# Optimization experiments

Measured on AMD Instinct MI355X. Metric: run time of the kernel, lower is better.

Reference implementation:

```python
import jax, jax.numpy as jnp
import numpy as np


def setup_inputs() -> dict:
    key = jax.random.key(0)
    k1, k2 = jax.random.split(key)
    B, C, H, W = 64, 64, 32, 32
    ROWS, COLS, O, KH, KW = 28, 28, 128, 5, 5
    x = jax.random.normal(k1, (B, C, H, W), dtype=jnp.float32)
    weight = jax.random.normal(k2, (ROWS, COLS, O, C, KH, KW), dtype=jnp.float32) * 0.05
    return {"x": x, "weight": weight}


def reference(x, weight):
    # Locally-connected conv (unshared weights), stride 1, no padding.
    # output[b,o,i,j] = sum_{c,u,v} x[b,c,i+u,j+v] * weight[i,j,o,c,u,v]
    rows, cols, O, C, kh, kw = weight.shape
    # patches: [B, C, kh, kw, rows, cols] built from kh*kw shifted views (small fixed loop)
    patches = jnp.stack(
        [jnp.stack([x[:, :, u:u + rows, v:v + cols] for v in range(kw)], axis=2)
         for u in range(kh)], axis=2)
    return jnp.einsum('bcuvij,ijocuv->boij', patches, weight)
```

## Files before the change

kernel.cpp:

```cpp
#include <hip/hip_runtime.h>


typedef __attribute__((ext_vector_type(8))) short bf16x8;
typedef __attribute__((ext_vector_type(4))) float f32x4;
typedef unsigned int u32;
typedef unsigned short u16;

__device__ __forceinline__ u16 f2bf(float f) {
    u32 u = __float_as_uint(f);
    u = (u + 0x7fffu + ((u >> 16) & 1u)) >> 16;
    return (u16)u;
}

template<int DJ>
__device__ __forceinline__ void run_block(const float* __restrict__ xb,
                                          const float* __restrict__ wrow,
                                          float* __restrict__ outp,
                                          u16* As0, u16* As1,
                                          int tb, int q, int l15, int quad) {
    constexpr int KC = 160;

    auto build = [&](int cb, u16* dstbuf) {
        u16 bu[40];
#pragma unroll
        for (int half = 0; half < 2; ++half) {
            float fr[4][8];
#pragma unroll
            for (int rw = 0; rw < 4; ++rw) {
                const int R = cb * 32 + q * 8 + half * 4 + rw;
                const int c = R / 5, u = R - 5 * c;
                const float* p = xb + c * 1024 + u * 32;
                *(f32x4*)&fr[rw][0] = *(const f32x4*)(p);
                *(f32x4*)&fr[rw][4] = *(const f32x4*)(p + 4);
            }
#pragma unroll
            for (int rw = 0; rw < 4; ++rw)
#pragma unroll
                for (int v = 0; v < 5; ++v)
                    bu[(half * 4 + rw) * 5 + v] = f2bf(fr[rw][DJ + v]);
        }
        u16* dst = dstbuf + tb * KC + q * 40;
#pragma unroll
        for (int r = 0; r < 5; ++r)
            *(uint4*)(dst + r * 8) = *(const uint4*)&bu[r * 8];
    };

    f32x4 acc[4];
#pragma unroll
    for (int mt = 0; mt < 4; ++mt) acc[mt] = (f32x4)0.f;

    build(0, As0);
    __syncthreads();

    for (int cb = 0; cb < 10; ++cb) {
        const float* wc = wrow + cb * 160;
        f32x4 wr[10];
#pragma unroll
        for (int ks = 0; ks < 5; ++ks) {
            wr[2 * ks]     = *(const f32x4*)(wc + ks * 32);
            wr[2 * ks + 1] = *(const f32x4*)(wc + ks * 32 + 4);
        }
        if (cb < 9) build(cb + 1, (cb & 1) ? As0 : As1);

        const u16* A = (cb & 1) ? As1 : As0;
#pragma unroll
        for (int ks = 0; ks < 5; ++ks) {
            f32x4 w0 = wr[2 * ks], w1 = wr[2 * ks + 1];
            bf16x8 bv;
            bv[0] = (short)f2bf(w0[0]); bv[1] = (short)f2bf(w0[1]);
            bv[2] = (short)f2bf(w0[2]); bv[3] = (short)f2bf(w0[3]);
            bv[4] = (short)f2bf(w1[0]); bv[5] = (short)f2bf(w1[1]);
            bv[6] = (short)f2bf(w1[2]); bv[7] = (short)f2bf(w1[3]);
#pragma unroll
            for (int mt = 0; mt < 4; ++mt) {
                bf16x8 av = *(const bf16x8*)&A[(mt * 16 + l15) * KC + ks * 32 + quad * 8];
                acc[mt] = __builtin_amdgcn_mfma_f32_16x16x32_bf16(av, bv, acc[mt], 0, 0, 0);
            }
        }
        if (cb < 9) __syncthreads();
    }

#pragma unroll
    for (int mt = 0; mt < 4; ++mt)
#pragma unroll
        for (int r = 0; r < 4; ++r) {
            const int b = mt * 16 + quad * 4 + r;
            outp[(size_t)b * 100352] = acc[mt][r];
        }
}

__global__ __launch_bounds__(256, 3) void lconv_fused(const float* __restrict__ x,
                                                      const float* __restrict__ wgt,
                                                      float* __restrict__ out) {
    __shared__ u16 As[2][64 * 160];

    const int bx = blockIdx.x;
    const int s  = (bx >> 3) & 1;
    const int bq = (bx & 7) | ((bx >> 4) << 3);
    const int g  = (bq & 7) * 98 + (bq >> 3);
    const int i = g / 28, j = g - i * 28;
    const int j0 = j & ~3;

    const int t = threadIdx.x, lane = t & 63, wv = t >> 6;
    const int l15 = lane & 15, quad = lane >> 4;
    const int tb = t >> 2, q = t & 3;

    const float* xb = x + tb * 65536 + i * 32 + j0;
    const float* wrow = wgt + (size_t)g * 204800
                      + (size_t)(s * 64 + wv * 16 + l15) * 1600 + quad * 8;
    const int o = s * 64 + wv * 16 + l15;
    float* outp = out + (size_t)o * 784 + g;

    switch (j & 3) {
        case 0:  run_block<0>(xb, wrow, outp, &As[0][0], &As[1][0], tb, q, l15, quad); break;
        case 1:  run_block<1>(xb, wrow, outp, &As[0][0], &As[1][0], tb, q, l15, quad); break;
        case 2:  run_block<2>(xb, wrow, outp, &As[0][0], &As[1][0], tb, q, l15, quad); break;
        default: run_block<3>(xb, wrow, outp, &As[0][0], &As[1][0], tb, q, l15, quad); break;
    }
}

extern "C" void kernel_launch(void* const* d_in, const int* in_sizes, int n_in,
                              void* d_out, int out_size, void* d_ws, size_t ws_size,
                              hipStream_t stream) {
    const float* x   = (const float*)d_in[0];
    const float* wgt = (const float*)d_in[1];
    float* out       = (float*)d_out;
    (void)d_ws; (void)ws_size;
    lconv_fused<<<1568, 256, 0, stream>>>(x, wgt, out);
}
```

Baseline: 1.015 ms.

## Register-prefetch next chunk of x and weights, pad LDS rows

```diff
diff --git a/kernel.cpp b/kernel.cpp
--- a/kernel.cpp
+++ b/kernel.cpp
@@ -12,72 +12,110 @@
     return (u16)u;
 }
 
-template<int DJ>
-__device__ __forceinline__ void run_block(const float* __restrict__ xb,
-                                          const float* __restrict__ wrow,
-                                          float* __restrict__ outp,
-                                          u16* As0, u16* As1,
-                                          int tb, int q, int l15, int quad) {
-    constexpr int KC = 160;
+__device__ __forceinline__ f32x4 load4u(const float* p) {
+    f32x4 v; __builtin_memcpy(&v, p, 16); return v;
+}
 
-    auto build = [&](int cb, u16* dstbuf) {
+constexpr int KC  = 160;
+constexpr int LDK = 168;
+
+struct XReg { f32x4 a[8]; float b[8]; };
+struct WReg { f32x4 w[10]; };
+
+__global__ __launch_bounds__(256, 3) void lconv_fused(const float* __restrict__ x,
+                                                      const float* __restrict__ wgt,
+                                                      float* __restrict__ out) {
+    __shared__ u16 As[2][64 * LDK];
+
+    const int bx = blockIdx.x;
+    const int s  = (bx >> 3) & 1;
+    const int bq = (bx & 7) | ((bx >> 4) << 3);
+    const int g  = (bq & 7) * 98 + (bq >> 3);
+    const int i = g / 28, j = g - i * 28;
+
+    const int t = threadIdx.x, lane = t & 63, wv = t >> 6;
+    const int l15 = lane & 15, quad = lane >> 4;
+    const int tb = t >> 2, q = t & 3;
+
+    const float* xb = x + tb * 65536 + i * 32 + j;
+    const int o = s * 64 + wv * 16 + l15;
+    const float* wrow = wgt + (size_t)g * 204800 + (size_t)o * 1600 + quad * 8;
+    float* outp = out + (size_t)o * 784 + g;
+
+    auto loadX = [&](int cb, XReg& r) {
+#pragma unroll
+        for (int rw = 0; rw < 8; ++rw) {
+            const int R = cb * 32 + q * 8 + rw;
+            const int c = R / 5, u = R - 5 * c;
+            const float* p = xb + c * 1024 + u * 32;
+            r.a[rw] = load4u(p);
+            r.b[rw] = p[4];
+        }
+    };
+    auto loadW = [&](int cb, WReg& r) {
+        const float* wc = wrow + cb * 160;
+#pragma unroll
+        for (int ks = 0; ks < 5; ++ks) {
+            r.w[2 * ks]     = *(const f32x4*)(wc + ks * 32);
+            r.w[2 * ks + 1] = *(const f32x4*)(wc + ks * 32 + 4);
+        }
+    };
+    auto cvtW = [&](const WReg& r, bf16x8* bw) {
+#pragma unroll
+        for (int ks = 0; ks < 5; ++ks) {
+            const f32x4 w0 = r.w[2 * ks], w1 = r.w[2 * ks + 1];
+            bf16x8 bv;
+            bv[0] = (short)f2bf(w0[0]); bv[1] = (short)f2bf(w0[1]);
+            bv[2] = (short)f2bf(w0[2]); bv[3] = (short)f2bf(w0[3]);
+            bv[4] = (short)f2bf(w1[0]); bv[5] = (short)f2bf(w1[1]);
+            bv[6] = (short)f2bf(w1[2]); bv[7] = (short)f2bf(w1[3]);
+            bw[ks] = bv;
+        }
+    };
+    auto writeA = [&](const XReg& r, u16* dstbuf) {
         u16 bu[40];
 #pragma unroll
-        for (int half = 0; half < 2; ++half) {
-            float fr[4][8];
+        for (int rw = 0; rw < 8; ++rw) {
 #pragma unroll
-            for (int rw = 0; rw < 4; ++rw) {
-                const int R = cb * 32 + q * 8 + half * 4 + rw;
-                const int c = R / 5, u = R - 5 * c;
-                const float* p = xb + c * 1024 + u * 32;
-                *(f32x4*)&fr[rw][0] = *(const f32x4*)(p);
-                *(f32x4*)&fr[rw][4] = *(const f32x4*)(p + 4);
-            }
+            for (int v = 0; v < 4; ++v) bu[rw * 5 + v] = f2bf(r.a[rw][v]);
+            bu[rw * 5 + 4] = f2bf(r.b[rw]);
+        }
+        u16* dst = dstbuf + tb * LDK + q * 40;
 #pragma unroll
-            for (int rw = 0; rw < 4; ++rw)
-#pragma unroll
-                for (int v = 0; v < 5; ++v)
-                    bu[(half * 4 + rw) * 5 + v] = f2bf(fr[rw][DJ + v]);
-        }
-        u16* dst = dstbuf + tb * KC + q * 40;
-#pragma unroll
-        for (int r = 0; r < 5; ++r)
-            *(uint4*)(dst + r * 8) = *(const uint4*)&bu[r * 8];
+        for (int e = 0; e < 5; ++e)
+            *(uint4*)(dst + e * 8) = *(const uint4*)&bu[e * 8];
     };
 
     f32x4 acc[4];
 #pragma unroll
     for (int mt = 0; mt < 4; ++mt) acc[mt] = (f32x4)0.f;
 
-    build(0, As0);
-    __syncthreads();
-
-    for (int cb = 0; cb < 10; ++cb) {
-        const float* wc = wrow + cb * 160;
-        f32x4 wr[10];
+    auto mfmaPhase = [&](const u16* A, const bf16x8* bw) {
 #pragma unroll
-        for (int ks = 0; ks < 5; ++ks) {
-            wr[2 * ks]     = *(const f32x4*)(wc + ks * 32);
-            wr[2 * ks + 1] = *(const f32x4*)(wc + ks * 32 + 4);
-        }
-        if (cb < 9) build(cb + 1, (cb & 1) ? As0 : As1);
-
-        const u16* A = (cb & 1) ? As1 : As0;
-#pragma unroll
-        for (int ks = 0; ks < 5; ++ks) {
-            f32x4 w0 = wr[2 * ks], w1 = wr[2 * ks + 1];
-            bf16x8 bv;
-            bv[0] = (short)f2bf(w0[0]); bv[1] = (short)f2bf(w0[1]);
-            bv[2] = (short)f2bf(w0[2]); bv[3] = (short)f2bf(w0[3]);
-            bv[4] = (short)f2bf(w1[0]); bv[5] = (short)f2bf(w1[1]);
-            bv[6] = (short)f2bf(w1[2]); bv[7] = (short)f2bf(w1[3]);
+        for (int ks = 0; ks < 5; ++ks)
 #pragma unroll
             for (int mt = 0; mt < 4; ++mt) {
-                bf16x8 av = *(const bf16x8*)&A[(mt * 16 + l15) * KC + ks * 32 + quad * 8];
-                acc[mt] = __builtin_amdgcn_mfma_f32_16x16x32_bf16(av, bv, acc[mt], 0, 0, 0);
+                bf16x8 av = *(const bf16x8*)&A[(mt * 16 + l15) * LDK + ks * 32 + quad * 8];
+                acc[mt] = __builtin_amdgcn_mfma_f32_16x16x32_bf16(av, bw[ks], acc[mt], 0, 0, 0);
             }
-        }
-        if (cb < 9) __syncthreads();
+    };
+
+    XReg xA, xB; WReg wA, wB; bf16x8 bw[5];
+    loadW(0, wA); loadX(0, xA);
+
+    for (int p = 0; p < 5; ++p) {
+        const int cb = 2 * p;
+        cvtW(wA, bw);
+        writeA(xA, As[0]);
+        loadW(cb + 1, wB); loadX(cb + 1, xB);
+        __syncthreads();
+        mfmaPhase(As[0], bw);
+
+        cvtW(wB, bw);
+        writeA(xB, As[1]);
+        if (p < 4) { loadW(cb + 2, wA); loadX(cb + 2, xA); }
+        __syncthreads();
+        mfmaPhase(As[1], bw);
     }
 
 #pragma unroll
@@ -89,36 +127,6 @@
         }
 }
 
-__global__ __launch_bounds__(256, 3) void lconv_fused(const float* __restrict__ x,
-                                                      const float* __restrict__ wgt,
-                                                      float* __restrict__ out) {
-    __shared__ u16 As[2][64 * 160];
-
-    const int bx = blockIdx.x;
-    const int s  = (bx >> 3) & 1;
-    const int bq = (bx & 7) | ((bx >> 4) << 3);
-    const int g  = (bq & 7) * 98 + (bq >> 3);
-    const int i = g / 28, j = g - i * 28;
-    const int j0 = j & ~3;
-
-    const int t = threadIdx.x, lane = t & 63, wv = t >> 6;
-    const int l15 = lane & 15, quad = lane >> 4;
-    const int tb = t >> 2, q = t & 3;
-
-    const float* xb = x + tb * 65536 + i * 32 + j0;
-    const float* wrow = wgt + (size_t)g * 204800
-                      + (size_t)(s * 64 + wv * 16 + l15) * 1600 + quad * 8;
-    const int o = s * 64 + wv * 16 + l15;
-    float* outp = out + (size_t)o * 784 + g;
-
-    switch (j & 3) {
-        case 0:  run_block<0>(xb, wrow, outp, &As[0][0], &As[1][0], tb, q, l15, quad); break;
-        case 1:  run_block<1>(xb, wrow, outp, &As[0][0], &As[1][0], tb, q, l15, quad); break;
-        case 2:  run_block<2>(xb, wrow, outp, &As[0][0], &As[1][0], tb, q, l15, quad); break;
-        default: run_block<3>(xb, wrow, outp, &As[0][0], &As[1][0], tb, q, l15, quad); break;
-    }
-}
-
 extern "C" void kernel_launch(void* const* d_in, const int* in_sizes, int n_in,
                               void* d_out, int out_size, void* d_ws, size_t ws_size,
                               hipStream_t stream) {
```

After: 1.161 ms. +14.4%, slower.
